# Kernel tuning notes

Measured on AMD Instinct MI355X. Metric: run time of the kernel, lower is better.

## Reference

```python
import math
import jax, jax.numpy as jnp
import numpy as np

NUM_PARAM = 5
STRIDE = 1
BN_EPS = 1e-5


def _get_pn(num_param):
    # Base kernel sampling offsets (non-negative grid, like the torch _get_p_n)
    base = round(math.sqrt(num_param))
    row = num_param // base
    mod = num_param % base
    gx, gy = np.meshgrid(np.arange(row), np.arange(base), indexing='ij')
    px, py = gx.ravel(), gy.ravel()
    if mod > 0:
        px = np.concatenate([px, np.full(mod, row)])
        py = np.concatenate([py, np.arange(mod)])
    return px.astype(np.float32), py.astype(np.float32)


def setup_inputs() -> dict:
    key = jax.random.key(0)
    ks = jax.random.split(key, 8)
    B, C1, C2, H, W, n = 8, 128, 256, 80, 80, NUM_PARAM
    x = jax.random.normal(ks[0], (B, C1, H, W), dtype=jnp.float32)
    # small offset-predictor weights so sampled positions stay moderate
    pw = jax.random.normal(ks[1], (2 * n, C1, 3, 3), dtype=jnp.float32) * 0.01
    pb = jax.random.normal(ks[2], (2 * n,), dtype=jnp.float32) * 0.01
    cw = jax.random.normal(ks[3], (C2, C1, n, 1), dtype=jnp.float32) * 0.05
    bn_gamma = jax.random.uniform(ks[4], (C2,), dtype=jnp.float32) + 0.5
    bn_beta = jax.random.normal(ks[5], (C2,), dtype=jnp.float32) * 0.1
    bn_mean = jax.random.normal(ks[6], (C2,), dtype=jnp.float32) * 0.1
    bn_var = jax.random.uniform(ks[7], (C2,), dtype=jnp.float32) + 0.5
    return {"x": x, "pw": pw, "pb": pb, "cw": cw,
            "bn_gamma": bn_gamma, "bn_beta": bn_beta,
            "bn_mean": bn_mean, "bn_var": bn_var}


def reference(x, pw, pb, cw, bn_gamma, bn_beta, bn_mean, bn_var):
    B, C, H, W = x.shape
    n = NUM_PARAM
    # offset predictor: 3x3 conv, padding 1, stride STRIDE -> [B, 2n, Ho, Wo]
    offset = jax.lax.conv_general_dilated(
        x, pw, window_strides=(STRIDE, STRIDE), padding=((1, 1), (1, 1)),
        dimension_numbers=('NCHW', 'OIHW', 'NCHW')) + pb[None, :, None, None]
    Ho, Wo = offset.shape[2], offset.shape[3]

    pn_x, pn_y = _get_pn(n)
    grid_x = (jnp.arange(Ho, dtype=x.dtype) * STRIDE)[:, None]  # [Ho,1]
    grid_y = (jnp.arange(Wo, dtype=x.dtype) * STRIDE)[None, :]  # [1,Wo]
    # sampling positions [B, n, Ho, Wo]
    px = offset[:, :n] + grid_x[None, None] + jnp.asarray(pn_x)[None, :, None, None]
    py = offset[:, n:] + grid_y[None, None] + jnp.asarray(pn_y)[None, :, None, None]

    pf = jax.lax.stop_gradient(jnp.floor(px))
    qf = jax.lax.stop_gradient(jnp.floor(py))
    qx_lt = jnp.clip(pf, 0, H - 1)
    qy_lt = jnp.clip(qf, 0, W - 1)
    qx_rb = jnp.clip(pf + 1, 0, H - 1)
    qy_rb = jnp.clip(qf + 1, 0, W - 1)

    pxc = jnp.clip(px, 0, H - 1)
    pyc = jnp.clip(py, 0, W - 1)

    g_lt = (1 + (qx_lt - pxc)) * (1 + (qy_lt - pyc))
    g_rb = (1 - (qx_rb - pxc)) * (1 - (qy_rb - pyc))
    g_lb = (1 + (qx_lt - pxc)) * (1 - (qy_rb - pyc))
    g_rt = (1 - (qx_rb - pxc)) * (1 + (qy_lt - pyc))

    x_flat = x.reshape(B, C, H * W)

    def gather(qx, qy):
        idx = (qx * W + qy).astype(jnp.int32).reshape(B, 1, -1)  # [B,1,n*Ho*Wo]
        out = jnp.take_along_axis(x_flat, jnp.broadcast_to(idx, (B, C, idx.shape[-1])), axis=2)
        return out.reshape(B, C, n, Ho, Wo)

    x_off = (g_lt[:, None] * gather(qx_lt, qy_lt)
             + g_rb[:, None] * gather(qx_rb, qy_rb)
             + g_lb[:, None] * gather(qx_lt, qy_rb)
             + g_rt[:, None] * gather(qx_rb, qy_lt))  # [B,C,n,Ho,Wo]

    # reshape to [B, C, Ho*n, Wo] (matches torch permute(0,1,2,4,3).view)
    x_off = x_off.transpose(0, 1, 3, 2, 4).reshape(B, C, Ho * n, Wo)

    y = jax.lax.conv_general_dilated(
        x_off, cw, window_strides=(n, 1), padding='VALID',
        dimension_numbers=('NCHW', 'OIHW', 'NCHW'))  # [B,C2,Ho,Wo]
    # BatchNorm (eval) + SiLU
    inv = bn_gamma / jnp.sqrt(bn_var + BN_EPS)
    y = (y - bn_mean[None, :, None, None]) * inv[None, :, None, None] + bn_beta[None, :, None, None]
    return y * jax.nn.sigmoid(y)
```

## Files before the change

### kernel.cpp

```cpp
#include <hip/hip_runtime.h>
#include <hip/hip_bf16.h>


typedef __attribute__((ext_vector_type(8))) short short8;
typedef __attribute__((ext_vector_type(4))) float f32x4;

#define Bsz 8
#define C1 128
#define C2 256
#define HW 6400
#define NP 5

#define NPOS (Bsz*NP*HW)
#define WS_IDX4 0
#define WS_WGT4 (WS_IDX4 + NPOS*16)
#define WS_XT   (WS_WGT4 + NPOS*16)
#define WS_XTLO (WS_XT + Bsz*HW*C1*2)
#define WS_ACW  (WS_XTLO + Bsz*HW*C1*2)
#define WS_APWH (WS_ACW + C2*C1*NP*2)
#define WS_APWL (WS_APWH + 18432*2)
#define WS_BNS  (WS_APWL + 18432*2)
#define WS_BNT  (WS_BNS + 1024)

__device__ __forceinline__ unsigned short f2bf(float f) {
  __hip_bfloat16 h = __float2bfloat16(f);
  return reinterpret_cast<unsigned short&>(h);
}
__device__ __forceinline__ float bfu2f(unsigned short u) {
  unsigned int v = ((unsigned int)u) << 16;
  return reinterpret_cast<float&>(v);
}

__global__ __launch_bounds__(256) void k_pre(
    const float* __restrict__ cw, const float* __restrict__ pw,
    const float* __restrict__ gam, const float* __restrict__ bet,
    const float* __restrict__ mu, const float* __restrict__ var,
    unsigned short* __restrict__ acw, unsigned short* __restrict__ apwh,
    unsigned short* __restrict__ apwl,
    float* __restrict__ bns, float* __restrict__ bnt) {
  int i = blockIdx.x * 256 + threadIdx.x;
  if (i < 163840) {
    int j = i & 7, lane = (i >> 3) & 63, mtile = (i >> 9) & 15;
    int cc = (i >> 13) & 3, k = i >> 15;
    int m = mtile * 16 + (lane & 15);
    int c = cc * 32 + (lane >> 4) * 8 + j;
    acw[i] = f2bf(cw[(m * C1 + c) * NP + k]);
  } else {
    int i2 = i - 163840;
    int j = i2 & 7, lane = (i2 >> 3) & 63, chunk = i2 >> 9;
    int m = lane & 15, tap = chunk >> 2;
    int c = (chunk & 3) * 32 + (lane >> 4) * 8 + j;
    float wv = (m < 10) ? pw[(m * C1 + c) * 9 + tap] : 0.f;
    unsigned short hi = f2bf(wv);
    apwh[i2] = hi;
    apwl[i2] = f2bf(wv - bfu2f(hi));
  }
  if (blockIdx.x == 0) {
    int t = threadIdx.x;
    float s = gam[t] * rsqrtf(var[t] + 1e-5f);
    bns[t] = s;
    bnt[t] = bet[t] - mu[t] * s;
  }
}

__global__ __launch_bounds__(256) void k_trans(const float* __restrict__ x,
                                               unsigned short* __restrict__ xT,
                                               unsigned short* __restrict__ xTlo) {
  __shared__ float lds[128][33];
  int t = threadIdx.x;
  int gp0 = blockIdx.x * 32;
  int b = gp0 / HW, p0 = gp0 - b * HW;
  const float* xb = x + (size_t)b * C1 * HW;
  int q = t & 7, r = t >> 3;
#pragma unroll
  for (int pass = 0; pass < 4; ++pass) {
    int c = pass * 32 + r;
    float4 v = *(const float4*)(xb + (size_t)c * HW + p0 + q * 4);
    lds[c][q * 4 + 0] = v.x;
    lds[c][q * 4 + 1] = v.y;
    lds[c][q * 4 + 2] = v.z;
    lds[c][q * 4 + 3] = v.w;
  }
  __syncthreads();
  int px = t >> 3, u = t & 7;
#pragma unroll
  for (int it = 0; it < 2; ++it) {
    int unit = it * 8 + u;
    int c0 = unit * 8;
    unsigned short vh[8], vl[8];
#pragma unroll
    for (int e = 0; e < 8; ++e) {
      float f = lds[c0 + e][px];
      unsigned short h = f2bf(f);
      vh[e] = h;
      vl[e] = f2bf(f - bfu2f(h));
    }
    size_t base = (size_t)(gp0 + px) * C1 + unit * 8;
    *(uint4*)(xT + base) = *(uint4*)vh;
    *(uint4*)(xTlo + base) = *(uint4*)vl;
  }
}

__global__ __launch_bounds__(64) void k_offset(
    const unsigned short* __restrict__ xT, const unsigned short* __restrict__ xTlo,
    const unsigned short* __restrict__ apwh, const unsigned short* __restrict__ apwl,
    const float* __restrict__ pb,
    int4* __restrict__ idx4, float4* __restrict__ wgt4) {
  __shared__ float sOff[10][16];
  int t = threadIdx.x, lane = t;
  int n16 = lane & 15, koct = lane >> 4;
  int gp = blockIdx.x * 16 + n16;
  int b = gp / HW, p = gp - b * HW;
  int h = p / 80, w = p - h * 80;
  const char* xTb = (const char*)xT + (size_t)b * HW * 256;
  const char* xTlb = (const char*)xTlo + (size_t)b * HW * 256;

  f32x4 acc = (f32x4)(0.f);
#pragma unroll
  for (int chunk = 0; chunk < 36; ++chunk) {
    int tap = chunk >> 2, cc = chunk & 3;
    int dh = tap / 3 - 1, dw = tap - (tap / 3) * 3 - 1;
    int hh = h + dh, ww = w + dw;
    bool ok = ((unsigned)hh < 80u) && ((unsigned)ww < 80u);
    short8 bh = 0, bl = 0;
    if (ok) {
      int boff = ((hh * 80 + ww) << 8) + cc * 64 + koct * 16;
      bh = *(const short8*)(xTb + boff);
      bl = *(const short8*)(xTlb + boff);
    }
    short8 ah = *(const short8*)(apwh + (chunk * 64 + lane) * 8);
    short8 al = *(const short8*)(apwl + (chunk * 64 + lane) * 8);
    acc = __builtin_amdgcn_mfma_f32_16x16x32_bf16(ah, bh, acc, 0, 0, 0);
    acc = __builtin_amdgcn_mfma_f32_16x16x32_bf16(ah, bl, acc, 0, 0, 0);
    acc = __builtin_amdgcn_mfma_f32_16x16x32_bf16(al, bh, acc, 0, 0, 0);
  }

  int quad = lane >> 4;
#pragma unroll
  for (int r = 0; r < 4; ++r) {
    int row = quad * 4 + r;
    if (row < 10) sOff[row][n16] = acc[r];
  }
  __syncthreads();

  for (int task = t; task < 80; task += 64) {
    int k = task >> 4, n = task & 15;
    int gp2 = blockIdx.x * 16 + n;
    int b2 = gp2 / HW, p2 = gp2 - b2 * HW;
    int h2 = p2 / 80, w2 = p2 - h2 * 80;
    float px = sOff[k][n] + pb[k] + (float)(h2 + (k >> 1));
    float py = sOff[5 + k][n] + pb[5 + k] + (float)(w2 + (k & 1));
    float pf = floorf(px), qf = floorf(py);
    float x0 = fminf(fmaxf(pf, 0.f), 79.f);
    float x1 = fminf(fmaxf(pf + 1.f, 0.f), 79.f);
    float y0 = fminf(fmaxf(qf, 0.f), 79.f);
    float y1 = fminf(fmaxf(qf + 1.f, 0.f), 79.f);
    float pxc = fminf(fmaxf(px, 0.f), 79.f);
    float pyc = fminf(fmaxf(py, 0.f), 79.f);
    float wx0 = 1.f + (x0 - pxc), wx1 = 1.f - (x1 - pxc);
    float wy0 = 1.f + (y0 - pyc), wy1 = 1.f - (y1 - pyc);
    int ix0 = (int)x0, ix1 = (int)x1, iy0 = (int)y0, iy1 = (int)y1;
    int g = (b2 * NP + k) * HW + p2;
    idx4[g] = make_int4((ix0 * 80 + iy0) << 8, (ix1 * 80 + iy1) << 8,
                        (ix0 * 80 + iy1) << 8, (ix1 * 80 + iy0) << 8);
    wgt4[g] = make_float4(wx0 * wy0, wx1 * wy1, wx0 * wy1, wx1 * wy0);
  }
}

__device__ __forceinline__ void stage_load(
    const char* xTb, const int4* __restrict__ idx4, const float4* __restrict__ wgt4,
    size_t sampBase, int k, int grp, int cchalf, int lane,
    uint4 q[2][4], float4& wg) {
  int p4 = lane & 15, j = lane >> 4;
  size_t g = sampBase + (size_t)k * HW + grp * 16 + p4;
  int4 id = idx4[g];
  wg = wgt4[g];
  int cj = j * 16;
#pragma unroll
  for (int hf = 0; hf < 2; ++hf) {
    int cb = (cchalf * 2 + hf) * 64 + cj;
    q[hf][0] = *(const uint4*)(xTb + id.x + cb);
    q[hf][1] = *(const uint4*)(xTb + id.y + cb);
    q[hf][2] = *(const uint4*)(xTb + id.z + cb);
    q[hf][3] = *(const uint4*)(xTb + id.w + cb);
  }
}

__device__ __forceinline__ void stage_store(
    unsigned short* BsBuf, int grp, int cchalf, int lane,
    uint4 q[2][4], float4 wg) {
#pragma unroll
  for (int hf = 0; hf < 2; ++hf) {
    int cc = cchalf * 2 + hf;
    const unsigned short* a0 = (const unsigned short*)&q[hf][0];
    const unsigned short* a1 = (const unsigned short*)&q[hf][1];
    const unsigned short* a2 = (const unsigned short*)&q[hf][2];
    const unsigned short* a3 = (const unsigned short*)&q[hf][3];
    union { uint4 v; unsigned short u[8]; } rr;
#pragma unroll
    for (int e = 0; e < 8; ++e) {
      float f = wg.x * bfu2f(a0[e]) + wg.y * bfu2f(a1[e])
              + wg.z * bfu2f(a2[e]) + wg.w * bfu2f(a3[e]);
      rr.u[e] = f2bf(f);
    }
    *(uint4*)&BsBuf[((cc * 2 + grp) * 64 + lane) * 8] = rr.v;
  }
}

__global__ __launch_bounds__(256) void k_main(
    const unsigned short* __restrict__ xT,
    const unsigned short* __restrict__ acw,
    const int4* __restrict__ idx4, const float4* __restrict__ wgt4,
    const float* __restrict__ bns, const float* __restrict__ bnt,
    float* __restrict__ out) {
  __shared__ unsigned short Bs[2][8 * 64 * 8];

  int t = threadIdx.x;
  int gp0 = blockIdx.x * 32;
  int b = gp0 / HW, pbase = gp0 - b * HW;
  int wave = t >> 6, lane = t & 63;
  int grp = wave & 1, cchalf = wave >> 1;
  const char* xTb = (const char*)xT + (size_t)b * HW * 256;
  size_t sampBase = (size_t)b * NP * HW + pbase;

  f32x4 acc[4][2];
#pragma unroll
  for (int mt = 0; mt < 4; ++mt)
#pragma unroll
    for (int nt = 0; nt < 2; ++nt) acc[mt][nt] = (f32x4)(0.f);

  uint4 pf[2][4];
  float4 pwg;
  stage_load(xTb, idx4, wgt4, sampBase, 0, grp, cchalf, lane, pf, pwg);
  stage_store(Bs[0], grp, cchalf, lane, pf, pwg);

#pragma unroll
  for (int k = 0; k < NP; ++k) {
    __syncthreads();
    if (k + 1 < NP)
      stage_load(xTb, idx4, wgt4, sampBase, k + 1, grp, cchalf, lane, pf, pwg);
    const unsigned short* Bk = Bs[k & 1];
#pragma unroll
    for (int cc = 0; cc < 4; ++cc) {
      short8 bfr[2];
#pragma unroll
      for (int nt = 0; nt < 2; ++nt)
        bfr[nt] = *(const short8*)&Bk[((cc * 2 + nt) * 64 + lane) * 8];
      const unsigned short* ab =
          acw + (size_t)((((k * 4 + cc) * 16) + wave * 4) * 64 + lane) * 8;
#pragma unroll
      for (int mt = 0; mt < 4; ++mt) {
        short8 a = *(const short8*)(ab + mt * 64 * 8);
#pragma unroll
        for (int nt = 0; nt < 2; ++nt)
          acc[mt][nt] = __builtin_amdgcn_mfma_f32_16x16x32_bf16(
              a, bfr[nt], acc[mt][nt], 0, 0, 0);
      }
    }
    if (k + 1 < NP)
      stage_store(Bs[(k + 1) & 1], grp, cchalf, lane, pf, pwg);
  }

  int quad = lane >> 4, col = lane & 15;
#pragma unroll
  for (int mt = 0; mt < 4; ++mt) {
    int m0 = wave * 64 + mt * 16 + quad * 4;
#pragma unroll
    for (int r = 0; r < 4; ++r) {
      int m = m0 + r;
      float s = bns[m], sh = bnt[m];
      float* op = out + ((size_t)(b * C2 + m)) * HW + pbase;
#pragma unroll
      for (int nt = 0; nt < 2; ++nt) {
        float y = fmaf(acc[mt][nt][r], s, sh);
        op[nt * 16 + col] = y * (1.f / (1.f + __expf(-y)));
      }
    }
  }
}

extern "C" void kernel_launch(void* const* d_in, const int* in_sizes, int n_in,
                              void* d_out, int out_size, void* d_ws, size_t ws_size,
                              hipStream_t stream) {
  const float* x  = (const float*)d_in[0];
  const float* pw = (const float*)d_in[1];
  const float* pb = (const float*)d_in[2];
  const float* cw = (const float*)d_in[3];
  const float* bg = (const float*)d_in[4];
  const float* bb = (const float*)d_in[5];
  const float* bm = (const float*)d_in[6];
  const float* bv = (const float*)d_in[7];
  float* out = (float*)d_out;

  char* ws = (char*)d_ws;
  int4*           idx4 = (int4*)(ws + WS_IDX4);
  float4*         wgt4 = (float4*)(ws + WS_WGT4);
  unsigned short* xT   = (unsigned short*)(ws + WS_XT);
  unsigned short* xTlo = (unsigned short*)(ws + WS_XTLO);
  unsigned short* acw  = (unsigned short*)(ws + WS_ACW);
  unsigned short* apwh = (unsigned short*)(ws + WS_APWH);
  unsigned short* apwl = (unsigned short*)(ws + WS_APWL);
  float*          bns  = (float*)(ws + WS_BNS);
  float*          bnt  = (float*)(ws + WS_BNT);

  k_pre<<<712, 256, 0, stream>>>(cw, pw, bg, bb, bm, bv, acw, apwh, apwl, bns, bnt);
  k_trans<<<1600, 256, 0, stream>>>(x, xT, xTlo);
  k_offset<<<3200, 64, 0, stream>>>(xT, xTlo, apwh, apwl, pb, idx4, wgt4);
  k_main<<<1600, 256, 0, stream>>>(xT, acw, idx4, wgt4, bns, bnt, out);
}
```

Baseline: 198.0 us.

## Merge prep and transpose kernels; make main kernel single-wave with no LDS

Folds the weight-prep and x-transpose kernels into one launch, with the block index choosing the role, which saves one kernel launch. The main kernel changes from a 4-wave block that shares bilinear-gathered tiles through double-buffered LDS into a single 64-thread wave. That wave gathers its own B fragments into registers and computes all 256 output channels, holding 32 accumulators per lane. This removes LDS traffic and barriers but gives only one wave per block. It raises register pressure and lowers the latency hiding that the old staged prefetch provided.

```diff
diff --git a/kernel.cpp b/kernel.cpp
--- a/kernel.cpp
+++ b/kernel.cpp
@@ -31,44 +31,43 @@
   return reinterpret_cast<float&>(v);
 }
 
-__global__ __launch_bounds__(256) void k_pre(
-    const float* __restrict__ cw, const float* __restrict__ pw,
+__global__ __launch_bounds__(256) void k_prep(
+    const float* __restrict__ x, const float* __restrict__ cw,
+    const float* __restrict__ pw,
     const float* __restrict__ gam, const float* __restrict__ bet,
     const float* __restrict__ mu, const float* __restrict__ var,
+    unsigned short* __restrict__ xT, unsigned short* __restrict__ xTlo,
     unsigned short* __restrict__ acw, unsigned short* __restrict__ apwh,
     unsigned short* __restrict__ apwl,
     float* __restrict__ bns, float* __restrict__ bnt) {
-  int i = blockIdx.x * 256 + threadIdx.x;
-  if (i < 163840) {
-    int j = i & 7, lane = (i >> 3) & 63, mtile = (i >> 9) & 15;
-    int cc = (i >> 13) & 3, k = i >> 15;
-    int m = mtile * 16 + (lane & 15);
-    int c = cc * 32 + (lane >> 4) * 8 + j;
-    acw[i] = f2bf(cw[(m * C1 + c) * NP + k]);
-  } else {
-    int i2 = i - 163840;
-    int j = i2 & 7, lane = (i2 >> 3) & 63, chunk = i2 >> 9;
-    int m = lane & 15, tap = chunk >> 2;
-    int c = (chunk & 3) * 32 + (lane >> 4) * 8 + j;
-    float wv = (m < 10) ? pw[(m * C1 + c) * 9 + tap] : 0.f;
-    unsigned short hi = f2bf(wv);
-    apwh[i2] = hi;
-    apwl[i2] = f2bf(wv - bfu2f(hi));
-  }
-  if (blockIdx.x == 0) {
-    int t = threadIdx.x;
-    float s = gam[t] * rsqrtf(var[t] + 1e-5f);
-    bns[t] = s;
-    bnt[t] = bet[t] - mu[t] * s;
-  }
-}
-
-__global__ __launch_bounds__(256) void k_trans(const float* __restrict__ x,
-                                               unsigned short* __restrict__ xT,
-                                               unsigned short* __restrict__ xTlo) {
   __shared__ float lds[128][33];
   int t = threadIdx.x;
-  int gp0 = blockIdx.x * 32;
+  if (blockIdx.x < 712) {
+    int i = blockIdx.x * 256 + t;
+    if (i < 163840) {
+      int j = i & 7, lane = (i >> 3) & 63, mtile = (i >> 9) & 15;
+      int cc = (i >> 13) & 3, k = i >> 15;
+      int m = mtile * 16 + (lane & 15);
+      int c = cc * 32 + (lane >> 4) * 8 + j;
+      acw[i] = f2bf(cw[(m * C1 + c) * NP + k]);
+    } else {
+      int i2 = i - 163840;
+      int j = i2 & 7, lane = (i2 >> 3) & 63, chunk = i2 >> 9;
+      int m = lane & 15, tap = chunk >> 2;
+      int c = (chunk & 3) * 32 + (lane >> 4) * 8 + j;
+      float wv = (m < 10) ? pw[(m * C1 + c) * 9 + tap] : 0.f;
+      unsigned short hi = f2bf(wv);
+      apwh[i2] = hi;
+      apwl[i2] = f2bf(wv - bfu2f(hi));
+    }
+    if (blockIdx.x == 0) {
+      float s = gam[t] * rsqrtf(var[t] + 1e-5f);
+      bns[t] = s;
+      bnt[t] = bet[t] - mu[t] * s;
+    }
+    return;
+  }
+  int gp0 = (blockIdx.x - 712) * 32;
   int b = gp0 / HW, p0 = gp0 - b * HW;
   const float* xb = x + (size_t)b * C1 * HW;
   int q = t & 7, r = t >> 3;
@@ -167,107 +166,74 @@
   }
 }
 
-__device__ __forceinline__ void stage_load(
-    const char* xTb, const int4* __restrict__ idx4, const float4* __restrict__ wgt4,
-    size_t sampBase, int k, int grp, int cchalf, int lane,
-    uint4 q[2][4], float4& wg) {
-  int p4 = lane & 15, j = lane >> 4;
-  size_t g = sampBase + (size_t)k * HW + grp * 16 + p4;
-  int4 id = idx4[g];
-  wg = wgt4[g];
-  int cj = j * 16;
-#pragma unroll
-  for (int hf = 0; hf < 2; ++hf) {
-    int cb = (cchalf * 2 + hf) * 64 + cj;
-    q[hf][0] = *(const uint4*)(xTb + id.x + cb);
-    q[hf][1] = *(const uint4*)(xTb + id.y + cb);
-    q[hf][2] = *(const uint4*)(xTb + id.z + cb);
-    q[hf][3] = *(const uint4*)(xTb + id.w + cb);
-  }
-}
-
-__device__ __forceinline__ void stage_store(
-    unsigned short* BsBuf, int grp, int cchalf, int lane,
-    uint4 q[2][4], float4 wg) {
-#pragma unroll
-  for (int hf = 0; hf < 2; ++hf) {
-    int cc = cchalf * 2 + hf;
-    const unsigned short* a0 = (const unsigned short*)&q[hf][0];
-    const unsigned short* a1 = (const unsigned short*)&q[hf][1];
-    const unsigned short* a2 = (const unsigned short*)&q[hf][2];
-    const unsigned short* a3 = (const unsigned short*)&q[hf][3];
-    union { uint4 v; unsigned short u[8]; } rr;
-#pragma unroll
-    for (int e = 0; e < 8; ++e) {
-      float f = wg.x * bfu2f(a0[e]) + wg.y * bfu2f(a1[e])
-              + wg.z * bfu2f(a2[e]) + wg.w * bfu2f(a3[e]);
-      rr.u[e] = f2bf(f);
-    }
-    *(uint4*)&BsBuf[((cc * 2 + grp) * 64 + lane) * 8] = rr.v;
-  }
-}
-
-__global__ __launch_bounds__(256) void k_main(
+__global__ __launch_bounds__(64) void k_main(
     const unsigned short* __restrict__ xT,
     const unsigned short* __restrict__ acw,
     const int4* __restrict__ idx4, const float4* __restrict__ wgt4,
     const float* __restrict__ bns, const float* __restrict__ bnt,
     float* __restrict__ out) {
-  __shared__ unsigned short Bs[2][8 * 64 * 8];
-
-  int t = threadIdx.x;
+  int lane = threadIdx.x;
   int gp0 = blockIdx.x * 32;
   int b = gp0 / HW, pbase = gp0 - b * HW;
-  int wave = t >> 6, lane = t & 63;
-  int grp = wave & 1, cchalf = wave >> 1;
+  int n16 = lane & 15, koct = lane >> 4;
   const char* xTb = (const char*)xT + (size_t)b * HW * 256;
   size_t sampBase = (size_t)b * NP * HW + pbase;
 
-  f32x4 acc[4][2];
-#pragma unroll
-  for (int mt = 0; mt < 4; ++mt)
-#pragma unroll
-    for (int nt = 0; nt < 2; ++nt) acc[mt][nt] = (f32x4)(0.f);
-
-  uint4 pf[2][4];
-  float4 pwg;
-  stage_load(xTb, idx4, wgt4, sampBase, 0, grp, cchalf, lane, pf, pwg);
-  stage_store(Bs[0], grp, cchalf, lane, pf, pwg);
+  f32x4 acc[16][2];
+#pragma unroll
+  for (int mt = 0; mt < 16; ++mt) {
+    acc[mt][0] = (f32x4)(0.f);
+    acc[mt][1] = (f32x4)(0.f);
+  }
 
 #pragma unroll
   for (int k = 0; k < NP; ++k) {
-    __syncthreads();
-    if (k + 1 < NP)
-      stage_load(xTb, idx4, wgt4, sampBase, k + 1, grp, cchalf, lane, pf, pwg);
-    const unsigned short* Bk = Bs[k & 1];
+    int4 id[2];
+    float4 wg[2];
+#pragma unroll
+    for (int nt = 0; nt < 2; ++nt) {
+      size_t g = sampBase + (size_t)k * HW + nt * 16 + n16;
+      id[nt] = idx4[g];
+      wg[nt] = wgt4[g];
+    }
 #pragma unroll
     for (int cc = 0; cc < 4; ++cc) {
+      int cb = cc * 64 + koct * 16;
       short8 bfr[2];
 #pragma unroll
-      for (int nt = 0; nt < 2; ++nt)
-        bfr[nt] = *(const short8*)&Bk[((cc * 2 + nt) * 64 + lane) * 8];
+      for (int nt = 0; nt < 2; ++nt) {
+        union { uint4 v; unsigned short u[8]; } q0, q1, q2, q3, rr;
+        q0.v = *(const uint4*)(xTb + id[nt].x + cb);
+        q1.v = *(const uint4*)(xTb + id[nt].y + cb);
+        q2.v = *(const uint4*)(xTb + id[nt].z + cb);
+        q3.v = *(const uint4*)(xTb + id[nt].w + cb);
+#pragma unroll
+        for (int e = 0; e < 8; ++e) {
+          float f = wg[nt].x * bfu2f(q0.u[e]) + wg[nt].y * bfu2f(q1.u[e])
+                  + wg[nt].z * bfu2f(q2.u[e]) + wg[nt].w * bfu2f(q3.u[e]);
+          rr.u[e] = f2bf(f);
+        }
+        bfr[nt] = *(short8*)&rr;
+      }
       const unsigned short* ab =
-          acw + (size_t)((((k * 4 + cc) * 16) + wave * 4) * 64 + lane) * 8;
-#pragma unroll
-      for (int mt = 0; mt < 4; ++mt) {
-        short8 a = *(const short8*)(ab + mt * 64 * 8);
-#pragma unroll
-        for (int nt = 0; nt < 2; ++nt)
-          acc[mt][nt] = __builtin_amdgcn_mfma_f32_16x16x32_bf16(
-              a, bfr[nt], acc[mt][nt], 0, 0, 0);
+          acw + ((size_t)((k * 4 + cc) * 16) * 64 + lane) * 8;
+#pragma unroll
+      for (int mt = 0; mt < 16; ++mt) {
+        short8 a = *(const short8*)(ab + (size_t)mt * 64 * 8);
+        acc[mt][0] = __builtin_amdgcn_mfma_f32_16x16x32_bf16(
+            a, bfr[0], acc[mt][0], 0, 0, 0);
+        acc[mt][1] = __builtin_amdgcn_mfma_f32_16x16x32_bf16(
+            a, bfr[1], acc[mt][1], 0, 0, 0);
       }
     }
-    if (k + 1 < NP)
-      stage_store(Bs[(k + 1) & 1], grp, cchalf, lane, pf, pwg);
   }
 
   int quad = lane >> 4, col = lane & 15;
 #pragma unroll
-  for (int mt = 0; mt < 4; ++mt) {
-    int m0 = wave * 64 + mt * 16 + quad * 4;
+  for (int mt = 0; mt < 16; ++mt) {
 #pragma unroll
     for (int r = 0; r < 4; ++r) {
-      int m = m0 + r;
+      int m = mt * 16 + quad * 4 + r;
       float s = bns[m], sh = bnt[m];
       float* op = out + ((size_t)(b * C2 + m)) * HW + pbase;
 #pragma unroll
@@ -303,8 +269,8 @@
   float*          bns  = (float*)(ws + WS_BNS);
   float*          bnt  = (float*)(ws + WS_BNT);
 
-  k_pre<<<712, 256, 0, stream>>>(cw, pw, bg, bb, bm, bv, acw, apwh, apwl, bns, bnt);
-  k_trans<<<1600, 256, 0, stream>>>(x, xT, xTlo);
+  k_prep<<<2312, 256, 0, stream>>>(x, cw, pw, bg, bb, bm, bv,
+                                   xT, xTlo, acw, apwh, apwl, bns, bnt);
   k_offset<<<3200, 64, 0, stream>>>(xT, xTlo, apwh, apwl, pb, idx4, wgt4);
-  k_main<<<1600, 256, 0, stream>>>(xT, acw, idx4, wgt4, bns, bnt, out);
-}
+  k_main<<<1600, 64, 0, stream>>>(xT, acw, idx4, wgt4, bns, bnt, out);
+}
```

Result: slower. 215.9 us (+9.1%).

## Stage 3x3 conv input patch in LDS and merge prep kernels

Applied to the files above, without the earlier changes.

The offset-predictor kernel now runs 4 waves per block over a 4x16 output tile. It stages an 18x6 halo patch of hi/lo bf16 channels in shared memory per channel chunk, so the nine taps reuse one copy instead of each wave issuing overlapping global loads. Separately, the weight-preparation and input-transpose kernels are folded into one launch, with the block range deciding which job a block does, which saves a kernel launch. The cost is added __syncthreads per channel chunk and extra LDS use, which may lower occupancy.

```diff
diff --git a/kernel.cpp b/kernel.cpp
--- a/kernel.cpp
+++ b/kernel.cpp
@@ -31,44 +31,43 @@
   return reinterpret_cast<float&>(v);
 }
 
-__global__ __launch_bounds__(256) void k_pre(
-    const float* __restrict__ cw, const float* __restrict__ pw,
+__global__ __launch_bounds__(256) void k_prep(
+    const float* __restrict__ x, const float* __restrict__ cw,
+    const float* __restrict__ pw,
     const float* __restrict__ gam, const float* __restrict__ bet,
     const float* __restrict__ mu, const float* __restrict__ var,
+    unsigned short* __restrict__ xT, unsigned short* __restrict__ xTlo,
     unsigned short* __restrict__ acw, unsigned short* __restrict__ apwh,
     unsigned short* __restrict__ apwl,
     float* __restrict__ bns, float* __restrict__ bnt) {
-  int i = blockIdx.x * 256 + threadIdx.x;
-  if (i < 163840) {
-    int j = i & 7, lane = (i >> 3) & 63, mtile = (i >> 9) & 15;
-    int cc = (i >> 13) & 3, k = i >> 15;
-    int m = mtile * 16 + (lane & 15);
-    int c = cc * 32 + (lane >> 4) * 8 + j;
-    acw[i] = f2bf(cw[(m * C1 + c) * NP + k]);
-  } else {
-    int i2 = i - 163840;
-    int j = i2 & 7, lane = (i2 >> 3) & 63, chunk = i2 >> 9;
-    int m = lane & 15, tap = chunk >> 2;
-    int c = (chunk & 3) * 32 + (lane >> 4) * 8 + j;
-    float wv = (m < 10) ? pw[(m * C1 + c) * 9 + tap] : 0.f;
-    unsigned short hi = f2bf(wv);
-    apwh[i2] = hi;
-    apwl[i2] = f2bf(wv - bfu2f(hi));
-  }
-  if (blockIdx.x == 0) {
-    int t = threadIdx.x;
-    float s = gam[t] * rsqrtf(var[t] + 1e-5f);
-    bns[t] = s;
-    bnt[t] = bet[t] - mu[t] * s;
-  }
-}
-
-__global__ __launch_bounds__(256) void k_trans(const float* __restrict__ x,
-                                               unsigned short* __restrict__ xT,
-                                               unsigned short* __restrict__ xTlo) {
   __shared__ float lds[128][33];
   int t = threadIdx.x;
-  int gp0 = blockIdx.x * 32;
+  if (blockIdx.x < 712) {
+    int i = blockIdx.x * 256 + t;
+    if (i < 163840) {
+      int j = i & 7, lane = (i >> 3) & 63, mtile = (i >> 9) & 15;
+      int cc = (i >> 13) & 3, k = i >> 15;
+      int m = mtile * 16 + (lane & 15);
+      int c = cc * 32 + (lane >> 4) * 8 + j;
+      acw[i] = f2bf(cw[(m * C1 + c) * NP + k]);
+    } else {
+      int i2 = i - 163840;
+      int j = i2 & 7, lane = (i2 >> 3) & 63, chunk = i2 >> 9;
+      int m = lane & 15, tap = chunk >> 2;
+      int c = (chunk & 3) * 32 + (lane >> 4) * 8 + j;
+      float wv = (m < 10) ? pw[(m * C1 + c) * 9 + tap] : 0.f;
+      unsigned short hi = f2bf(wv);
+      apwh[i2] = hi;
+      apwl[i2] = f2bf(wv - bfu2f(hi));
+    }
+    if (blockIdx.x == 0) {
+      float s = gam[t] * rsqrtf(var[t] + 1e-5f);
+      bns[t] = s;
+      bnt[t] = bet[t] - mu[t] * s;
+    }
+    return;
+  }
+  int gp0 = (blockIdx.x - 712) * 32;
   int b = gp0 / HW, p0 = gp0 - b * HW;
   const float* xb = x + (size_t)b * C1 * HW;
   int q = t & 7, r = t >> 3;
@@ -101,55 +100,69 @@
   }
 }
 
-__global__ __launch_bounds__(64) void k_offset(
+__global__ __launch_bounds__(256) void k_offset(
     const unsigned short* __restrict__ xT, const unsigned short* __restrict__ xTlo,
     const unsigned short* __restrict__ apwh, const unsigned short* __restrict__ apwl,
     const float* __restrict__ pb,
     int4* __restrict__ idx4, float4* __restrict__ wgt4) {
-  __shared__ float sOff[10][16];
-  int t = threadIdx.x, lane = t;
+  __shared__ __align__(16) char patch[2 * 6 * 18 * 80];
+  __shared__ float sOff[4][10][16];
+
+  int t = threadIdx.x, wave = t >> 6, lane = t & 63;
   int n16 = lane & 15, koct = lane >> 4;
-  int gp = blockIdx.x * 16 + n16;
-  int b = gp / HW, p = gp - b * HW;
-  int h = p / 80, w = p - h * 80;
-  const char* xTb = (const char*)xT + (size_t)b * HW * 256;
+  int blk = blockIdx.x;
+  int b = blk / 100;
+  int rem = blk - b * 100;
+  int h0 = (rem / 5) * 4, w0 = (rem % 5) * 16;
+  const char* xTb  = (const char*)xT  + (size_t)b * HW * 256;
   const char* xTlb = (const char*)xTlo + (size_t)b * HW * 256;
 
   f32x4 acc = (f32x4)(0.f);
 #pragma unroll
-  for (int chunk = 0; chunk < 36; ++chunk) {
-    int tap = chunk >> 2, cc = chunk & 3;
-    int dh = tap / 3 - 1, dw = tap - (tap / 3) * 3 - 1;
-    int hh = h + dh, ww = w + dw;
-    bool ok = ((unsigned)hh < 80u) && ((unsigned)ww < 80u);
-    short8 bh = 0, bl = 0;
-    if (ok) {
-      int boff = ((hh * 80 + ww) << 8) + cc * 64 + koct * 16;
-      bh = *(const short8*)(xTb + boff);
-      bl = *(const short8*)(xTlb + boff);
-    }
-    short8 ah = *(const short8*)(apwh + (chunk * 64 + lane) * 8);
-    short8 al = *(const short8*)(apwl + (chunk * 64 + lane) * 8);
-    acc = __builtin_amdgcn_mfma_f32_16x16x32_bf16(ah, bh, acc, 0, 0, 0);
-    acc = __builtin_amdgcn_mfma_f32_16x16x32_bf16(ah, bl, acc, 0, 0, 0);
-    acc = __builtin_amdgcn_mfma_f32_16x16x32_bf16(al, bh, acc, 0, 0, 0);
+  for (int cc = 0; cc < 4; ++cc) {
+    __syncthreads();
+    for (int u = t; u < 864; u += 256) {
+      int half = (u >= 432) ? 1 : 0;
+      int r2 = u - half * 432;
+      int unit = r2 & 3, slot = r2 >> 2;
+      int pr = slot / 18, pc = slot - pr * 18;
+      int r = h0 - 1 + pr, c = w0 - 1 + pc;
+      uint4 v = make_uint4(0u, 0u, 0u, 0u);
+      if (((unsigned)r < 80u) && ((unsigned)c < 80u)) {
+        const char* src = (half ? xTlb : xTb) + (((r * 80 + c) << 8) + cc * 64 + unit * 16);
+        v = *(const uint4*)src;
+      }
+      *(uint4*)(patch + half * 8640 + slot * 80 + unit * 16) = v;
+    }
+    __syncthreads();
+#pragma unroll
+    for (int tap = 0; tap < 9; ++tap) {
+      int dh = tap / 3, dw = tap - dh * 3;
+      int lo = (((wave + dh) * 18) + (n16 + dw)) * 80 + koct * 16;
+      short8 bh = *(const short8*)(patch + lo);
+      short8 bl = *(const short8*)(patch + 8640 + lo);
+      short8 ah = *(const short8*)(apwh + ((tap * 4 + cc) * 64 + lane) * 8);
+      short8 al = *(const short8*)(apwl + ((tap * 4 + cc) * 64 + lane) * 8);
+      acc = __builtin_amdgcn_mfma_f32_16x16x32_bf16(ah, bh, acc, 0, 0, 0);
+      acc = __builtin_amdgcn_mfma_f32_16x16x32_bf16(ah, bl, acc, 0, 0, 0);
+      acc = __builtin_amdgcn_mfma_f32_16x16x32_bf16(al, bh, acc, 0, 0, 0);
+    }
   }
 
   int quad = lane >> 4;
 #pragma unroll
   for (int r = 0; r < 4; ++r) {
     int row = quad * 4 + r;
-    if (row < 10) sOff[row][n16] = acc[r];
+    if (row < 10) sOff[wave][row][n16] = acc[r];
   }
   __syncthreads();
 
-  for (int task = t; task < 80; task += 64) {
-    int k = task >> 4, n = task & 15;
-    int gp2 = blockIdx.x * 16 + n;
-    int b2 = gp2 / HW, p2 = gp2 - b2 * HW;
-    int h2 = p2 / 80, w2 = p2 - h2 * 80;
-    float px = sOff[k][n] + pb[k] + (float)(h2 + (k >> 1));
-    float py = sOff[5 + k][n] + pb[5 + k] + (float)(w2 + (k & 1));
+  for (int task = t; task < 320; task += 256) {
+    int wv = task / 80, rem2 = task - wv * 80, k = rem2 >> 4, n = rem2 & 15;
+    int h2 = h0 + wv, w2 = w0 + n;
+    int p2 = h2 * 80 + w2;
+    float px = sOff[wv][k][n] + pb[k] + (float)(h2 + (k >> 1));
+    float py = sOff[wv][5 + k][n] + pb[5 + k] + (float)(w2 + (k & 1));
     float pf = floorf(px), qf = floorf(py);
     float x0 = fminf(fmaxf(pf, 0.f), 79.f);
     float x1 = fminf(fmaxf(pf + 1.f, 0.f), 79.f);
@@ -160,7 +173,7 @@
     float wx0 = 1.f + (x0 - pxc), wx1 = 1.f - (x1 - pxc);
     float wy0 = 1.f + (y0 - pyc), wy1 = 1.f - (y1 - pyc);
     int ix0 = (int)x0, ix1 = (int)x1, iy0 = (int)y0, iy1 = (int)y1;
-    int g = (b2 * NP + k) * HW + p2;
+    int g = (b * NP + k) * HW + p2;
     idx4[g] = make_int4((ix0 * 80 + iy0) << 8, (ix1 * 80 + iy1) << 8,
                         (ix0 * 80 + iy1) << 8, (ix1 * 80 + iy0) << 8);
     wgt4[g] = make_float4(wx0 * wy0, wx1 * wy1, wx0 * wy1, wx1 * wy0);
@@ -303,8 +316,8 @@
   float*          bns  = (float*)(ws + WS_BNS);
   float*          bnt  = (float*)(ws + WS_BNT);
 
-  k_pre<<<712, 256, 0, stream>>>(cw, pw, bg, bb, bm, bv, acw, apwh, apwl, bns, bnt);
-  k_trans<<<1600, 256, 0, stream>>>(x, xT, xTlo);
-  k_offset<<<3200, 64, 0, stream>>>(xT, xTlo, apwh, apwl, pb, idx4, wgt4);
+  k_prep<<<2312, 256, 0, stream>>>(x, cw, pw, bg, bb, bm, bv,
+                                   xT, xTlo, acw, apwh, apwl, bns, bnt);
+  k_offset<<<800, 256, 0, stream>>>(xT, xTlo, apwh, apwl, pb, idx4, wgt4);
   k_main<<<1600, 256, 0, stream>>>(xT, acw, idx4, wgt4, bns, bnt, out);
 }
```

After: 178.5 us. 9.8% less time.
